# Performance work log

Hardware: AMD Instinct MI355X
Metric: run time of the kernel (lower is better)

Reference implementation:

```python
import jax, jax.numpy as jnp
import numpy as np

N = 512          # nsites (even)
B = 1024         # batch of spin configurations
HALF = N // 2

# static off-diagonal scatter indices (~eye mask)
_ROWS, _COLS = np.nonzero(~np.eye(N, dtype=bool))


def setup_inputs() -> dict:
    key = jax.random.key(0)
    k_f, k_x = jax.random.split(key)
    scale = np.float32(np.sqrt(2.0 * np.e / N))
    F = jax.random.normal(k_f, (N * N - N,), jnp.float32) * scale
    # balanced +/-1 spins per sample (zero magnetization), random permutation per row
    base = jnp.concatenate([jnp.ones(HALF, jnp.float32), -jnp.ones(HALF, jnp.float32)])
    keys = jax.random.split(k_x, B)
    x = jax.vmap(lambda k: jax.random.permutation(k, base))(keys)
    return {"x": x, "F": F}


def reference(x, F):
    # scatter parameters into dense off-diagonal pair matrix (shared across batch)
    F_full = jnp.zeros((N, N), F.dtype).at[_ROWS, _COLS].set(F)

    def single(xs):
        # spin system: up occupation then down occupation -> exactly N particles
        occ = jnp.concatenate([xs > 0, xs <= 0])
        idx = jnp.flatnonzero(occ, size=N)          # [N] int
        up = idx[:HALF]                              # up-site indices in [0, N)
        dn = idx[HALF:] - N                          # down-site indices in [0, N)
        sub = F_full[up[:, None], dn[None, :]]       # [N/2, N/2] gathered submatrix
        return jnp.linalg.det(sub)

    return jax.vmap(single)(x)  # [B]
```

## Files before the change

kernel.cpp:

```cpp
#include <hip/hip_runtime.h>

#define NN 512
#define NM1 511
#define PCT(r, j) pcT[(r) * 13 + (j)]

#define T32(X, K) X(K,0) X(K,1) X(K,2) X(K,3) X(K,4) X(K,5) X(K,6) X(K,7) \
  X(K,8) X(K,9) X(K,10) X(K,11) X(K,12) X(K,13) X(K,14) X(K,15) \
  X(K,16) X(K,17) X(K,18) X(K,19) X(K,20) X(K,21) X(K,22) X(K,23) \
  X(K,24) X(K,25) X(K,26) X(K,27) X(K,28) X(K,29) X(K,30) X(K,31)
#define T4x32(X) T32(X,0) T32(X,1) T32(X,2) T32(X,3)
#define T32S(X) X(0) X(1) X(2) X(3) X(4) X(5) X(6) X(7) \
  X(8) X(9) X(10) X(11) X(12) X(13) X(14) X(15) \
  X(16) X(17) X(18) X(19) X(20) X(21) X(22) X(23) \
  X(24) X(25) X(26) X(27) X(28) X(29) X(30) X(31)
#define P8(X, K) X(K,0) X(K,1) X(K,2) X(K,3) X(K,4) X(K,5) X(K,6) X(K,7)
#define P4x8(X) P8(X,0) P8(X,1) P8(X,2) P8(X,3)

__device__ __forceinline__ float rdlane(float v, int l) {
  return __uint_as_float(
      (unsigned)__builtin_amdgcn_readlane((int)__float_as_uint(v), l));
}

__global__ __launch_bounds__(512, 2) void det_lu_kernel(
    const float* __restrict__ x,
    const float* __restrict__ F,
    float* __restrict__ out) {
  __shared__ __align__(16) float pcT[256 * 13];
  __shared__ __align__(16) float lbuf[8 * 256];
  __shared__ __align__(16) float Ubuf[8 * 260];
  __shared__ float livef[256];
  __shared__ int   perm[256];
  __shared__ int   upbuf[256];
  __shared__ int   dnbuf[256];
  __shared__ int   wavecnt[8];
  __shared__ int   totinv;
  __shared__ float ldspad[12100];

  const int tid = threadIdx.x;
  const int L   = tid & 63;
  const int w   = tid >> 6;

  const float* xrow = x + (size_t)blockIdx.x * NN;

  if ((int)blockIdx.x < 0) ((volatile float*)ldspad)[tid] = 1.0f;

  float xv = xrow[tid];
  bool pos = xv > 0.0f;
  unsigned long long mask = __ballot(pos);
  if (L == 0) wavecnt[w] = __popcll(mask);
  if (tid == 0) totinv = 0;
  if (tid < 256) livef[tid] = 1.0f;
  __syncthreads();
  {
    int base = 0;
    for (int i = 0; i < w; i++) base += wavecnt[i];
    int pbelow = __popcll(mask & ((1ull << L) - 1ull));
    if (pos) upbuf[base + pbelow] = tid;
    else     dnbuf[(64 * w - base) + (L - pbelow)] = tid;
  }
  __syncthreads();

#define DECLC(M) const int cg##M = dnbuf[32 * w + (M)];
  T32S(DECLC)
  const int rg0 = upbuf[L];
  const int rg1 = upbuf[L + 64];
  const int rg2 = upbuf[L + 128];
  const int rg3 = upbuf[L + 192];
#define DECLA(K, M)                                                         \
  float a##K##_##M = (cg##M == rg##K)                                       \
      ? 0.0f                                                                \
      : F[(size_t)rg##K * NM1 + cg##M - (cg##M > rg##K ? 1 : 0)];
  T4x32(DECLA)

  if (w == 0) {
#define S0(K, M) if ((M) < 8) PCT(L + 64 * (K), (M)) = a##K##_##M;
    T4x32(S0)
  }
  double det = 1.0;
  __syncthreads();

#define DPPMAX(CTRL) {                                                      \
    unsigned _t = (unsigned)__builtin_amdgcn_update_dpp(                    \
        0, (int)key, (CTRL), 0xf, 0xf, false);                              \
    key = key > _t ? key : _t; }
#define BCJ(K, J, S) if ((J) >= (S)) uv##J = rdlane(pr##K##_##J, lp);
#define BCARM(K, S)                                                         \
    if (kp == (K)) { BCJ(K,0,S) BCJ(K,1,S) BCJ(K,2,S) BCJ(K,3,S)            \
                     BCJ(K,4,S) BCJ(K,5,S) BCJ(K,6,S) BCJ(K,7,S) }
#define LSTEP(K, S)                                                         \
    float l##K = ((dead4 >> (K)) & 1u) ? 0.0f : pr##K##_##S * invp;         \
    pr##K##_##S = l##K;
#define UPD(K, J, S)                                                        \
    if ((J) > (S)) pr##K##_##J = fmaf(-l##K, uv##J, pr##K##_##J);
#define UPDJ(J, S) UPD(0,J,S) UPD(1,J,S) UPD(2,J,S) UPD(3,J,S)
#define STQ(K, Q, M0, M1, M2, M3)                                           \
    if (kp == (K)) *reinterpret_cast<float4*>(&Ubuf[sb + 4 * (Q)]) =        \
        make_float4(a##K##_##M0, a##K##_##M1, a##K##_##M2, a##K##_##M3);
#define STHK(K)                                                             \
    STQ(K,0,0,1,2,3) STQ(K,1,4,5,6,7) STQ(K,2,8,9,10,11)                    \
    STQ(K,3,12,13,14,15) STQ(K,4,16,17,18,19) STQ(K,5,20,21,22,23)          \
    STQ(K,6,24,25,26,27) STQ(K,7,28,29,30,31)
#define FSTEP(S) {                                                          \
    unsigned b0 = (dead4 & 1u) ? 0u                                         \
        : ((__float_as_uint(fabsf(pr0_##S)) & 0xFFFFFF00u) | (unsigned)L);  \
    unsigned b1 = (dead4 & 2u) ? 0u                                         \
        : ((__float_as_uint(fabsf(pr1_##S)) & 0xFFFFFF00u) | (unsigned)(L + 64)); \
    unsigned b2 = (dead4 & 4u) ? 0u                                         \
        : ((__float_as_uint(fabsf(pr2_##S)) & 0xFFFFFF00u) | (unsigned)(L + 128)); \
    unsigned b3 = (dead4 & 8u) ? 0u                                         \
        : ((__float_as_uint(fabsf(pr3_##S)) & 0xFFFFFF00u) | (unsigned)(L + 192)); \
    unsigned m01 = b0 > b1 ? b0 : b1, m23 = b2 > b3 ? b2 : b3;              \
    unsigned key = m01 > m23 ? m01 : m23;                                   \
    DPPMAX(0x111) DPPMAX(0x112) DPPMAX(0x114) DPPMAX(0x118)                 \
    DPPMAX(0x142) DPPMAX(0x143)                                             \
    const int pv = __builtin_amdgcn_readlane((int)key, 63) & 255;           \
    const int kp = pv >> 6, lp = pv & 63;                                   \
    if (lp == L) dead4 |= 1u << kp;                                         \
    float uv0 = 0.f, uv1 = 0.f, uv2 = 0.f, uv3 = 0.f;                       \
    float uv4 = 0.f, uv5 = 0.f, uv6 = 0.f, uv7 = 0.f;                       \
    BCARM(0,S) BCARM(1,S) BCARM(2,S) BCARM(3,S)                             \
    const float piv = uv##S;                                                \
    det *= (double)piv;                                                     \
    const float invp = 1.0f / piv;                                          \
    LSTEP(0,S) LSTEP(1,S) LSTEP(2,S) LSTEP(3,S)                             \
    UPDJ(0,S) UPDJ(1,S) UPDJ(2,S) UPDJ(3,S)                                 \
    UPDJ(4,S) UPDJ(5,S) UPDJ(6,S) UPDJ(7,S)                                 \
    if (w == 0) {                                                           \
      lbuf[(S) * 256 + L      ] = l0;                                       \
      lbuf[(S) * 256 + L +  64] = l1;                                       \
      lbuf[(S) * 256 + L + 128] = l2;                                       \
      lbuf[(S) * 256 + L + 192] = l3;                                       \
      if (L == lp) livef[pv] = 0.0f;                                        \
      if (L == 0) perm[P * 8 + (S)] = pv;                                   \
    }                                                                       \
    if ((4 * w + 3 > P) && L == lp) {                                       \
      const int sb = (S) * 260 + 32 * w;                                    \
      STHK(0) STHK(1) STHK(2) STHK(3)                                       \
    }                                                                       \
  }

#pragma unroll 1
  for (int P = 0; P < 32; P++) {
#define LDP(K, J) float pr##K##_##J = PCT(L + 64 * (K), (J));
    P4x8(LDP)
    unsigned dead4 = 0u;

    FSTEP(0) FSTEP(1) FSTEP(2) FSTEP(3)
    FSTEP(4) FSTEP(5) FSTEP(6) FSTEP(7)

    __syncthreads();

    if (tid < 256) {
      const int j = tid;
      float u[8];
#pragma unroll
      for (int t = 0; t < 8; t++) {
        int pt = perm[P * 8 + t];
        float acc = Ubuf[t * 260 + j];
#pragma unroll
        for (int s2 = 0; s2 < t; s2++) acc = fmaf(-lbuf[s2 * 256 + pt], u[s2], acc);
        u[t] = acc;
        Ubuf[t * 260 + j] = acc;
      }
    }
    __syncthreads();

#define TUROW(K, A, B, C, D)                                                \
    a##K##_##A = fmaf(-lk##K, uq.x, a##K##_##A);                            \
    a##K##_##B = fmaf(-lk##K, uq.y, a##K##_##B);                            \
    a##K##_##C = fmaf(-lk##K, uq.z, a##K##_##C);                            \
    a##K##_##D = fmaf(-lk##K, uq.w, a##K##_##D);
#define TUQ(A, B, C, D)                                                     \
    TUROW(0, A, B, C, D) TUROW(1, A, B, C, D)                               \
    TUROW(2, A, B, C, D) TUROW(3, A, B, C, D)
    if (4 * w + 3 > P) {
#pragma unroll 1
      for (int t = 0; t < 8; t++) {
        const int lb = t * 256 + L;
        const float lk0 = lbuf[lb];
        const float lk1 = lbuf[lb + 64];
        const float lk2 = lbuf[lb + 128];
        const float lk3 = lbuf[lb + 192];
        const float* ub = &Ubuf[t * 260 + 32 * w];
        { const float4 uq = *reinterpret_cast<const float4*>(ub + 0);
          TUQ(0, 1, 2, 3) }
        { const float4 uq = *reinterpret_cast<const float4*>(ub + 4);
          TUQ(4, 5, 6, 7) }
        { const float4 uq = *reinterpret_cast<const float4*>(ub + 8);
          TUQ(8, 9, 10, 11) }
        { const float4 uq = *reinterpret_cast<const float4*>(ub + 12);
          TUQ(12, 13, 14, 15) }
        { const float4 uq = *reinterpret_cast<const float4*>(ub + 16);
          TUQ(16, 17, 18, 19) }
        { const float4 uq = *reinterpret_cast<const float4*>(ub + 20);
          TUQ(20, 21, 22, 23) }
        { const float4 uq = *reinterpret_cast<const float4*>(ub + 24);
          TUQ(24, 25, 26, 27) }
        { const float4 uq = *reinterpret_cast<const float4*>(ub + 28);
          TUQ(28, 29, 30, 31) }
      }
    }
    {
      const int wstar = (P + 1) >> 2, h = (P + 1) & 3;
      if (P < 31 && w == wstar) {
        const float lv0 = livef[L];
        const float lv1 = livef[L + 64];
        const float lv2 = livef[L + 128];
        const float lv3 = livef[L + 192];
#define SEa(K, M) if ((M) < 8)                PCT(L + 64*(K), (M))      = a##K##_##M * lv##K;
#define SEb(K, M) if ((M) >= 8 && (M) < 16)   PCT(L + 64*(K), (M) - 8)  = a##K##_##M * lv##K;
#define SEc(K, M) if ((M) >= 16 && (M) < 24)  PCT(L + 64*(K), (M) - 16) = a##K##_##M * lv##K;
#define SEd(K, M) if ((M) >= 24)              PCT(L + 64*(K), (M) - 24) = a##K##_##M * lv##K;
        if (h == 0)      { T4x32(SEa) }
        else if (h == 1) { T4x32(SEb) }
        else if (h == 2) { T4x32(SEc) }
        else             { T4x32(SEd) }
      }
    }
    __syncthreads();
  }

  int myinv = 0;
  {
    const int i0 = tid & 255;
    const int cbase = (tid >> 8) * 128;
    const int pi = perm[i0];
#pragma unroll 8
    for (int j = 0; j < 128; j++) {
      int jj = cbase + j;
      if (jj > i0 && perm[jj] < pi) myinv++;
    }
  }
#pragma unroll
  for (int off = 32; off; off >>= 1) myinv += __shfl_xor(myinv, off);
  if (L == 0) atomicAdd(&totinv, myinv);
  __syncthreads();
  if (tid == 0) out[blockIdx.x] = (float)((totinv & 1) ? -det : det);
}

extern "C" void kernel_launch(void* const* d_in, const int* in_sizes, int n_in,
                              void* d_out, int out_size, void* d_ws, size_t ws_size,
                              hipStream_t stream) {
  const float* x = (const float*)d_in[0];
  const float* F = (const float*)d_in[1];
  float* out = (float*)d_out;
  const int B = out_size;
  hipLaunchKernelGGL(det_lu_kernel, dim3(B), dim3(512), 0, stream, x, F, out);
}
```

Baseline: 1.051 ms.

## Replace shared-memory U panel solve with in-register L-factor back-solve per wave

```diff
diff --git a/kernel.cpp b/kernel.cpp
--- a/kernel.cpp
+++ b/kernel.cpp
@@ -26,7 +26,6 @@
     const float* __restrict__ F,
     float* __restrict__ out) {
   __shared__ __align__(16) float pcT[256 * 13];
-  __shared__ __align__(16) float lbuf[8 * 256];
   __shared__ __align__(16) float Ubuf[8 * 260];
   __shared__ float livef[256];
   __shared__ int   perm[256];
@@ -34,7 +33,7 @@
   __shared__ int   dnbuf[256];
   __shared__ int   wavecnt[8];
   __shared__ int   totinv;
-  __shared__ float ldspad[12100];
+  __shared__ float ldspad[14100];
 
   const int tid = threadIdx.x;
   const int L   = tid & 63;
@@ -115,6 +114,7 @@
     DPPMAX(0x142) DPPMAX(0x143)                                             \
     const int pv = __builtin_amdgcn_readlane((int)key, 63) & 255;           \
     const int kp = pv >> 6, lp = pv & 63;                                   \
+    kp##S = kp; lp##S = lp;                                                 \
     if (lp == L) dead4 |= 1u << kp;                                         \
     float uv0 = 0.f, uv1 = 0.f, uv2 = 0.f, uv3 = 0.f;                       \
     float uv4 = 0.f, uv5 = 0.f, uv6 = 0.f, uv7 = 0.f;                       \
@@ -126,80 +126,119 @@
     UPDJ(0,S) UPDJ(1,S) UPDJ(2,S) UPDJ(3,S)                                 \
     UPDJ(4,S) UPDJ(5,S) UPDJ(6,S) UPDJ(7,S)                                 \
     if (w == 0) {                                                           \
-      lbuf[(S) * 256 + L      ] = l0;                                       \
-      lbuf[(S) * 256 + L +  64] = l1;                                       \
-      lbuf[(S) * 256 + L + 128] = l2;                                       \
-      lbuf[(S) * 256 + L + 192] = l3;                                       \
       if (L == lp) livef[pv] = 0.0f;                                        \
       if (L == 0) perm[P * 8 + (S)] = pv;                                   \
     }                                                                       \
-    if ((4 * w + 3 > P) && L == lp) {                                       \
+    if (trailing && L == lp) {                                              \
       const int sb = (S) * 260 + 32 * w;                                    \
       STHK(0) STHK(1) STHK(2) STHK(3)                                       \
     }                                                                       \
   }
 
+#define GC(K,T,S) c##T##_##S = rdlane(pr##K##_##T, lp##S);
+#define GC1(K) GC(K,0,1)
+#define GC2(K) GC(K,0,2) GC(K,1,2)
+#define GC3(K) GC(K,0,3) GC(K,1,3) GC(K,2,3)
+#define GC4(K) GC(K,0,4) GC(K,1,4) GC(K,2,4) GC(K,3,4)
+#define GC5(K) GC(K,0,5) GC(K,1,5) GC(K,2,5) GC(K,3,5) GC(K,4,5)
+#define GC6(K) GC(K,0,6) GC(K,1,6) GC(K,2,6) GC(K,3,6) GC(K,4,6) GC(K,5,6)
+#define GC7(K) GC(K,0,7) GC(K,1,7) GC(K,2,7) GC(K,3,7) GC(K,4,7) GC(K,5,7) GC(K,6,7)
+#define SELK(S, GCn)                                                        \
+    if      (kp##S == 0) { GCn(0) }                                         \
+    else if (kp##S == 1) { GCn(1) }                                         \
+    else if (kp##S == 2) { GCn(2) }                                         \
+    else                 { GCn(3) }
+
+#define LSOLVE(K)                                                           \
+    pr##K##_6 = fmaf(-pr##K##_7, c6_7, pr##K##_6);                          \
+    pr##K##_5 = fmaf(-pr##K##_6, c5_6, pr##K##_5);                          \
+    pr##K##_5 = fmaf(-pr##K##_7, c5_7, pr##K##_5);                          \
+    pr##K##_4 = fmaf(-pr##K##_5, c4_5, pr##K##_4);                          \
+    pr##K##_4 = fmaf(-pr##K##_6, c4_6, pr##K##_4);                          \
+    pr##K##_4 = fmaf(-pr##K##_7, c4_7, pr##K##_4);                          \
+    pr##K##_3 = fmaf(-pr##K##_4, c3_4, pr##K##_3);                          \
+    pr##K##_3 = fmaf(-pr##K##_5, c3_5, pr##K##_3);                          \
+    pr##K##_3 = fmaf(-pr##K##_6, c3_6, pr##K##_3);                          \
+    pr##K##_3 = fmaf(-pr##K##_7, c3_7, pr##K##_3);                          \
+    pr##K##_2 = fmaf(-pr##K##_3, c2_3, pr##K##_2);                          \
+    pr##K##_2 = fmaf(-pr##K##_4, c2_4, pr##K##_2);                          \
+    pr##K##_2 = fmaf(-pr##K##_5, c2_5, pr##K##_2);                          \
+    pr##K##_2 = fmaf(-pr##K##_6, c2_6, pr##K##_2);                          \
+    pr##K##_2 = fmaf(-pr##K##_7, c2_7, pr##K##_2);                          \
+    pr##K##_1 = fmaf(-pr##K##_2, c1_2, pr##K##_1);                          \
+    pr##K##_1 = fmaf(-pr##K##_3, c1_3, pr##K##_1);                          \
+    pr##K##_1 = fmaf(-pr##K##_4, c1_4, pr##K##_1);                          \
+    pr##K##_1 = fmaf(-pr##K##_5, c1_5, pr##K##_1);                          \
+    pr##K##_1 = fmaf(-pr##K##_6, c1_6, pr##K##_1);                          \
+    pr##K##_1 = fmaf(-pr##K##_7, c1_7, pr##K##_1);                          \
+    pr##K##_0 = fmaf(-pr##K##_1, c0_1, pr##K##_0);                          \
+    pr##K##_0 = fmaf(-pr##K##_2, c0_2, pr##K##_0);                          \
+    pr##K##_0 = fmaf(-pr##K##_3, c0_3, pr##K##_0);                          \
+    pr##K##_0 = fmaf(-pr##K##_4, c0_4, pr##K##_0);                          \
+    pr##K##_0 = fmaf(-pr##K##_5, c0_5, pr##K##_0);                          \
+    pr##K##_0 = fmaf(-pr##K##_6, c0_6, pr##K##_0);                          \
+    pr##K##_0 = fmaf(-pr##K##_7, c0_7, pr##K##_0);
+
+#define TUROW(K, T, A, B, C, D)                                             \
+    a##K##_##A = fmaf(-pr##K##_##T, uq.x, a##K##_##A);                      \
+    a##K##_##B = fmaf(-pr##K##_##T, uq.y, a##K##_##B);                      \
+    a##K##_##C = fmaf(-pr##K##_##T, uq.z, a##K##_##C);                      \
+    a##K##_##D = fmaf(-pr##K##_##T, uq.w, a##K##_##D);
+#define TUQn(T, A, B, C, D)                                                 \
+    TUROW(0, T, A, B, C, D) TUROW(1, T, A, B, C, D)                         \
+    TUROW(2, T, A, B, C, D) TUROW(3, T, A, B, C, D)
+#define TUT(T) {                                                            \
+    const float* ub = &Ubuf[(T) * 260 + 32 * w];                            \
+    { const float4 uq = *reinterpret_cast<const float4*>(ub + 0);           \
+      TUQn(T, 0, 1, 2, 3) }                                                 \
+    { const float4 uq = *reinterpret_cast<const float4*>(ub + 4);           \
+      TUQn(T, 4, 5, 6, 7) }                                                 \
+    { const float4 uq = *reinterpret_cast<const float4*>(ub + 8);           \
+      TUQn(T, 8, 9, 10, 11) }                                               \
+    { const float4 uq = *reinterpret_cast<const float4*>(ub + 12);          \
+      TUQn(T, 12, 13, 14, 15) }                                             \
+    { const float4 uq = *reinterpret_cast<const float4*>(ub + 16);          \
+      TUQn(T, 16, 17, 18, 19) }                                             \
+    { const float4 uq = *reinterpret_cast<const float4*>(ub + 20);          \
+      TUQn(T, 20, 21, 22, 23) }                                             \
+    { const float4 uq = *reinterpret_cast<const float4*>(ub + 24);          \
+      TUQn(T, 24, 25, 26, 27) }                                             \
+    { const float4 uq = *reinterpret_cast<const float4*>(ub + 28);          \
+      TUQn(T, 28, 29, 30, 31) }                                             \
+  }
+
 #pragma unroll 1
   for (int P = 0; P < 32; P++) {
-#define LDP(K, J) float pr##K##_##J = PCT(L + 64 * (K), (J));
-    P4x8(LDP)
-    unsigned dead4 = 0u;
-
-    FSTEP(0) FSTEP(1) FSTEP(2) FSTEP(3)
-    FSTEP(4) FSTEP(5) FSTEP(6) FSTEP(7)
+    const bool trailing  = (4 * w + 3 > P);
+    const bool factoring = trailing || (w == 0);
+    int kp1, lp1, kp2, lp2, kp3, lp3, kp4, lp4;
+    int kp5, lp5, kp6, lp6, kp7, lp7;
+    int kp0, lp0;
+    (void)kp0; (void)lp0;
+#define DPR(K, J) float pr##K##_##J;
+    P4x8(DPR)
+
+    if (factoring) {
+#define LDPA(K, J) pr##K##_##J = PCT(L + 64 * (K), (J));
+      P4x8(LDPA)
+      unsigned dead4 = 0u;
+      FSTEP(0) FSTEP(1) FSTEP(2) FSTEP(3)
+      FSTEP(4) FSTEP(5) FSTEP(6) FSTEP(7)
+    }
 
     __syncthreads();
 
-    if (tid < 256) {
-      const int j = tid;
-      float u[8];
-#pragma unroll
-      for (int t = 0; t < 8; t++) {
-        int pt = perm[P * 8 + t];
-        float acc = Ubuf[t * 260 + j];
-#pragma unroll
-        for (int s2 = 0; s2 < t; s2++) acc = fmaf(-lbuf[s2 * 256 + pt], u[s2], acc);
-        u[t] = acc;
-        Ubuf[t * 260 + j] = acc;
-      }
-    }
-    __syncthreads();
-
-#define TUROW(K, A, B, C, D)                                                \
-    a##K##_##A = fmaf(-lk##K, uq.x, a##K##_##A);                            \
-    a##K##_##B = fmaf(-lk##K, uq.y, a##K##_##B);                            \
-    a##K##_##C = fmaf(-lk##K, uq.z, a##K##_##C);                            \
-    a##K##_##D = fmaf(-lk##K, uq.w, a##K##_##D);
-#define TUQ(A, B, C, D)                                                     \
-    TUROW(0, A, B, C, D) TUROW(1, A, B, C, D)                               \
-    TUROW(2, A, B, C, D) TUROW(3, A, B, C, D)
-    if (4 * w + 3 > P) {
-#pragma unroll 1
-      for (int t = 0; t < 8; t++) {
-        const int lb = t * 256 + L;
-        const float lk0 = lbuf[lb];
-        const float lk1 = lbuf[lb + 64];
-        const float lk2 = lbuf[lb + 128];
-        const float lk3 = lbuf[lb + 192];
-        const float* ub = &Ubuf[t * 260 + 32 * w];
-        { const float4 uq = *reinterpret_cast<const float4*>(ub + 0);
-          TUQ(0, 1, 2, 3) }
-        { const float4 uq = *reinterpret_cast<const float4*>(ub + 4);
-          TUQ(4, 5, 6, 7) }
-        { const float4 uq = *reinterpret_cast<const float4*>(ub + 8);
-          TUQ(8, 9, 10, 11) }
-        { const float4 uq = *reinterpret_cast<const float4*>(ub + 12);
-          TUQ(12, 13, 14, 15) }
-        { const float4 uq = *reinterpret_cast<const float4*>(ub + 16);
-          TUQ(16, 17, 18, 19) }
-        { const float4 uq = *reinterpret_cast<const float4*>(ub + 20);
-          TUQ(20, 21, 22, 23) }
-        { const float4 uq = *reinterpret_cast<const float4*>(ub + 24);
-          TUQ(24, 25, 26, 27) }
-        { const float4 uq = *reinterpret_cast<const float4*>(ub + 28);
-          TUQ(28, 29, 30, 31) }
-      }
-    }
+    if (trailing) {
+      float c0_1, c0_2, c1_2, c0_3, c1_3, c2_3, c0_4, c1_4, c2_4, c3_4,
+            c0_5, c1_5, c2_5, c3_5, c4_5,
+            c0_6, c1_6, c2_6, c3_6, c4_6, c5_6,
+            c0_7, c1_7, c2_7, c3_7, c4_7, c5_7, c6_7;
+      SELK(1, GC1) SELK(2, GC2) SELK(3, GC3) SELK(4, GC4)
+      SELK(5, GC5) SELK(6, GC6) SELK(7, GC7)
+      LSOLVE(0) LSOLVE(1) LSOLVE(2) LSOLVE(3)
+      TUT(0) TUT(1) TUT(2) TUT(3) TUT(4) TUT(5) TUT(6) TUT(7)
+    }
+
     {
       const int wstar = (P + 1) >> 2, h = (P + 1) & 3;
       if (P < 31 && w == wstar) {
```

New measurement: 1.856 ms. 1.77x slower.

## Split LU columns across 16 waves with 16 columns each in 1024-thread blocks

Applied to the files above, without the earlier changes.

```diff
diff --git a/kernel.cpp b/kernel.cpp
--- a/kernel.cpp
+++ b/kernel.cpp
@@ -4,15 +4,11 @@
 #define NM1 511
 #define PCT(r, j) pcT[(r) * 13 + (j)]
 
-#define T32(X, K) X(K,0) X(K,1) X(K,2) X(K,3) X(K,4) X(K,5) X(K,6) X(K,7) \
-  X(K,8) X(K,9) X(K,10) X(K,11) X(K,12) X(K,13) X(K,14) X(K,15) \
-  X(K,16) X(K,17) X(K,18) X(K,19) X(K,20) X(K,21) X(K,22) X(K,23) \
-  X(K,24) X(K,25) X(K,26) X(K,27) X(K,28) X(K,29) X(K,30) X(K,31)
-#define T4x32(X) T32(X,0) T32(X,1) T32(X,2) T32(X,3)
-#define T32S(X) X(0) X(1) X(2) X(3) X(4) X(5) X(6) X(7) \
-  X(8) X(9) X(10) X(11) X(12) X(13) X(14) X(15) \
-  X(16) X(17) X(18) X(19) X(20) X(21) X(22) X(23) \
-  X(24) X(25) X(26) X(27) X(28) X(29) X(30) X(31)
+#define T16(X, K) X(K,0) X(K,1) X(K,2) X(K,3) X(K,4) X(K,5) X(K,6) X(K,7) \
+  X(K,8) X(K,9) X(K,10) X(K,11) X(K,12) X(K,13) X(K,14) X(K,15)
+#define T4x16(X) T16(X,0) T16(X,1) T16(X,2) T16(X,3)
+#define T16S(X) X(0) X(1) X(2) X(3) X(4) X(5) X(6) X(7) \
+  X(8) X(9) X(10) X(11) X(12) X(13) X(14) X(15)
 #define P8(X, K) X(K,0) X(K,1) X(K,2) X(K,3) X(K,4) X(K,5) X(K,6) X(K,7)
 #define P4x8(X) P8(X,0) P8(X,1) P8(X,2) P8(X,3)
 
@@ -21,7 +17,8 @@
       (unsigned)__builtin_amdgcn_readlane((int)__float_as_uint(v), l));
 }
 
-__global__ __launch_bounds__(512, 2) void det_lu_kernel(
+__global__ __attribute__((amdgpu_waves_per_eu(4, 4))) __launch_bounds__(1024)
+void det_lu_kernel(
     const float* __restrict__ x,
     const float* __restrict__ F,
     float* __restrict__ out) {
@@ -44,14 +41,18 @@
 
   if ((int)blockIdx.x < 0) ((volatile float*)ldspad)[tid] = 1.0f;
 
-  float xv = xrow[tid];
-  bool pos = xv > 0.0f;
-  unsigned long long mask = __ballot(pos);
-  if (L == 0) wavecnt[w] = __popcll(mask);
+  bool pos = false;
+  unsigned long long mask = 0;
+  if (tid < NN) {
+    float xv = xrow[tid];
+    pos = xv > 0.0f;
+    mask = __ballot(pos);
+    if (L == 0) wavecnt[w] = __popcll(mask);
+  }
   if (tid == 0) totinv = 0;
   if (tid < 256) livef[tid] = 1.0f;
   __syncthreads();
-  {
+  if (tid < NN) {
     int base = 0;
     for (int i = 0; i < w; i++) base += wavecnt[i];
     int pbelow = __popcll(mask & ((1ull << L) - 1ull));
@@ -60,8 +61,8 @@
   }
   __syncthreads();
 
-#define DECLC(M) const int cg##M = dnbuf[32 * w + (M)];
-  T32S(DECLC)
+#define DECLC(M) const int cg##M = dnbuf[16 * w + (M)];
+  T16S(DECLC)
   const int rg0 = upbuf[L];
   const int rg1 = upbuf[L + 64];
   const int rg2 = upbuf[L + 128];
@@ -70,11 +71,11 @@
   float a##K##_##M = (cg##M == rg##K)                                       \
       ? 0.0f                                                                \
       : F[(size_t)rg##K * NM1 + cg##M - (cg##M > rg##K ? 1 : 0)];
-  T4x32(DECLA)
+  T4x16(DECLA)
 
   if (w == 0) {
 #define S0(K, M) if ((M) < 8) PCT(L + 64 * (K), (M)) = a##K##_##M;
-    T4x32(S0)
+    T4x16(S0)
   }
   double det = 1.0;
   __syncthreads();
@@ -97,9 +98,8 @@
     if (kp == (K)) *reinterpret_cast<float4*>(&Ubuf[sb + 4 * (Q)]) =        \
         make_float4(a##K##_##M0, a##K##_##M1, a##K##_##M2, a##K##_##M3);
 #define STHK(K)                                                             \
-    STQ(K,0,0,1,2,3) STQ(K,1,4,5,6,7) STQ(K,2,8,9,10,11)                    \
-    STQ(K,3,12,13,14,15) STQ(K,4,16,17,18,19) STQ(K,5,20,21,22,23)          \
-    STQ(K,6,24,25,26,27) STQ(K,7,28,29,30,31)
+    STQ(K,0,0,1,2,3) STQ(K,1,4,5,6,7)                                       \
+    STQ(K,2,8,9,10,11) STQ(K,3,12,13,14,15)
 #define FSTEP(S) {                                                          \
     unsigned b0 = (dead4 & 1u) ? 0u                                         \
         : ((__float_as_uint(fabsf(pr0_##S)) & 0xFFFFFF00u) | (unsigned)L);  \
@@ -133,21 +133,33 @@
       if (L == lp) livef[pv] = 0.0f;                                        \
       if (L == 0) perm[P * 8 + (S)] = pv;                                   \
     }                                                                       \
-    if ((4 * w + 3 > P) && L == lp) {                                       \
-      const int sb = (S) * 260 + 32 * w;                                    \
+    if (trailing && L == lp) {                                              \
+      const int sb = (S) * 260 + 16 * w;                                    \
       STHK(0) STHK(1) STHK(2) STHK(3)                                       \
     }                                                                       \
   }
 
+#define TUROW(K, A, B, C, D)                                                \
+    a##K##_##A = fmaf(-lk##K, uq.x, a##K##_##A);                            \
+    a##K##_##B = fmaf(-lk##K, uq.y, a##K##_##B);                            \
+    a##K##_##C = fmaf(-lk##K, uq.z, a##K##_##C);                            \
+    a##K##_##D = fmaf(-lk##K, uq.w, a##K##_##D);
+#define TUQ(A, B, C, D)                                                     \
+    TUROW(0, A, B, C, D) TUROW(1, A, B, C, D)                               \
+    TUROW(2, A, B, C, D) TUROW(3, A, B, C, D)
+
 #pragma unroll 1
   for (int P = 0; P < 32; P++) {
+    const bool trailing  = (2 * w + 1 > P);
+    const bool factoring = trailing || (w == 0);
+
+    if (factoring) {
 #define LDP(K, J) float pr##K##_##J = PCT(L + 64 * (K), (J));
-    P4x8(LDP)
-    unsigned dead4 = 0u;
-
-    FSTEP(0) FSTEP(1) FSTEP(2) FSTEP(3)
-    FSTEP(4) FSTEP(5) FSTEP(6) FSTEP(7)
-
+      P4x8(LDP)
+      unsigned dead4 = 0u;
+      FSTEP(0) FSTEP(1) FSTEP(2) FSTEP(3)
+      FSTEP(4) FSTEP(5) FSTEP(6) FSTEP(7)
+    }
     __syncthreads();
 
     if (tid < 256) {
@@ -165,15 +177,7 @@
     }
     __syncthreads();
 
-#define TUROW(K, A, B, C, D)                                                \
-    a##K##_##A = fmaf(-lk##K, uq.x, a##K##_##A);                            \
-    a##K##_##B = fmaf(-lk##K, uq.y, a##K##_##B);                            \
-    a##K##_##C = fmaf(-lk##K, uq.z, a##K##_##C);                            \
-    a##K##_##D = fmaf(-lk##K, uq.w, a##K##_##D);
-#define TUQ(A, B, C, D)                                                     \
-    TUROW(0, A, B, C, D) TUROW(1, A, B, C, D)                               \
-    TUROW(2, A, B, C, D) TUROW(3, A, B, C, D)
-    if (4 * w + 3 > P) {
+    if (trailing) {
 #pragma unroll 1
       for (int t = 0; t < 8; t++) {
         const int lb = t * 256 + L;
@@ -181,7 +185,7 @@
         const float lk1 = lbuf[lb + 64];
         const float lk2 = lbuf[lb + 128];
         const float lk3 = lbuf[lb + 192];
-        const float* ub = &Ubuf[t * 260 + 32 * w];
+        const float* ub = &Ubuf[t * 260 + 16 * w];
         { const float4 uq = *reinterpret_cast<const float4*>(ub + 0);
           TUQ(0, 1, 2, 3) }
         { const float4 uq = *reinterpret_cast<const float4*>(ub + 4);
@@ -190,31 +194,19 @@
           TUQ(8, 9, 10, 11) }
         { const float4 uq = *reinterpret_cast<const float4*>(ub + 12);
           TUQ(12, 13, 14, 15) }
-        { const float4 uq = *reinterpret_cast<const float4*>(ub + 16);
-          TUQ(16, 17, 18, 19) }
-        { const float4 uq = *reinterpret_cast<const float4*>(ub + 20);
-          TUQ(20, 21, 22, 23) }
-        { const float4 uq = *reinterpret_cast<const float4*>(ub + 24);
-          TUQ(24, 25, 26, 27) }
-        { const float4 uq = *reinterpret_cast<const float4*>(ub + 28);
-          TUQ(28, 29, 30, 31) }
       }
     }
     {
-      const int wstar = (P + 1) >> 2, h = (P + 1) & 3;
+      const int wstar = (P + 1) >> 1, h = (P + 1) & 1;
       if (P < 31 && w == wstar) {
         const float lv0 = livef[L];
         const float lv1 = livef[L + 64];
         const float lv2 = livef[L + 128];
         const float lv3 = livef[L + 192];
-#define SEa(K, M) if ((M) < 8)                PCT(L + 64*(K), (M))      = a##K##_##M * lv##K;
-#define SEb(K, M) if ((M) >= 8 && (M) < 16)   PCT(L + 64*(K), (M) - 8)  = a##K##_##M * lv##K;
-#define SEc(K, M) if ((M) >= 16 && (M) < 24)  PCT(L + 64*(K), (M) - 16) = a##K##_##M * lv##K;
-#define SEd(K, M) if ((M) >= 24)              PCT(L + 64*(K), (M) - 24) = a##K##_##M * lv##K;
-        if (h == 0)      { T4x32(SEa) }
-        else if (h == 1) { T4x32(SEb) }
-        else if (h == 2) { T4x32(SEc) }
-        else             { T4x32(SEd) }
+#define SEa(K, M) if ((M) < 8)  PCT(L + 64*(K), (M))     = a##K##_##M * lv##K;
+#define SEb(K, M) if ((M) >= 8) PCT(L + 64*(K), (M) - 8) = a##K##_##M * lv##K;
+        if (h == 0) { T4x16(SEa) }
+        else        { T4x16(SEb) }
       }
     }
     __syncthreads();
@@ -223,10 +215,10 @@
   int myinv = 0;
   {
     const int i0 = tid & 255;
-    const int cbase = (tid >> 8) * 128;
+    const int cbase = (tid >> 8) * 64;
     const int pi = perm[i0];
 #pragma unroll 8
-    for (int j = 0; j < 128; j++) {
+    for (int j = 0; j < 64; j++) {
       int jj = cbase + j;
       if (jj > i0 && perm[jj] < pi) myinv++;
     }
@@ -245,5 +237,5 @@
   const float* F = (const float*)d_in[1];
   float* out = (float*)d_out;
   const int B = out_size;
-  hipLaunchKernelGGL(det_lu_kernel, dim3(B), dim3(512), 0, stream, x, F, out);
+  hipLaunchKernelGGL(det_lu_kernel, dim3(B), dim3(1024), 0, stream, x, F, out);
 }
```

Measured after the change: 977.4 us. 1.07x faster.
